# Performance work log

Hardware: AMD Instinct MI355X
Metric: run time of the kernel (lower is better)

The kernel has to match this reference:

```python
import jax, jax.numpy as jnp
import numpy as np

D_MODEL = 1024
EXPAND = 2
D_INNER = EXPAND * D_MODEL          # 2048
D_STATE = 64
NGROUPS = 1
HEADDIM = 128
NHEADS = D_INNER // HEADDIM         # 16
D_CONV = 4
CONV_DIM = D_INNER + 2 * NGROUPS * D_STATE      # 2176
D_IN_PROJ = 2 * D_INNER + 2 * NGROUPS * D_STATE + NHEADS  # 4240
BATCH = 2
SEQLEN = 4096
RMS_EPS = 1e-5


def setup_inputs() -> dict:
    key = jax.random.key(0)
    ks = jax.random.split(key, 8)
    u = jax.random.normal(ks[0], (BATCH, SEQLEN, D_MODEL), jnp.float32)
    in_proj_w = jax.random.normal(ks[1], (D_IN_PROJ, D_MODEL), jnp.float32) * 0.02
    conv_w = jax.random.normal(ks[2], (CONV_DIM, D_CONV), jnp.float32) * 0.2
    conv_b = jax.random.normal(ks[3], (CONV_DIM,), jnp.float32) * 0.1
    dt_bias = jax.random.normal(ks[4], (NHEADS,), jnp.float32) * 0.5
    # A ~ Uniform(1,16), A_log = log(A)  (as in Mamba2 init)
    A_log = jnp.log(jax.random.uniform(ks[5], (NHEADS,), jnp.float32, 1.0, 16.0))
    D = jnp.ones((NHEADS,), jnp.float32)
    rms_w = jnp.ones((D_INNER,), jnp.float32)
    out_w = jax.random.normal(ks[6], (D_MODEL, D_INNER), jnp.float32) * 0.02
    return {"u": u, "in_proj_w": in_proj_w, "conv_w": conv_w, "conv_b": conv_b,
            "dt_bias": dt_bias, "A_log": A_log, "D": D, "rms_w": rms_w, "out_w": out_w}


def reference(u, in_proj_w, conv_w, conv_b, dt_bias, A_log, D, rms_w, out_w):
    Bsz, L, _ = u.shape
    # in_proj: (B,L,d_model) -> (B,L,d_in_proj), split [z, x, B, C, dt]
    zxbcdt = jnp.einsum('bld,ed->ble', u, in_proj_w)
    s1 = D_INNER
    s2 = 2 * D_INNER
    s3 = s2 + NGROUPS * D_STATE
    s4 = s3 + NGROUPS * D_STATE
    z = zxbcdt[..., :s1]
    x = zxbcdt[..., s1:s2]
    B_part = zxbcdt[..., s2:s3]
    C_part = zxbcdt[..., s3:s4]
    dt = zxbcdt[..., s4:]
    dt = jax.nn.softplus(dt + dt_bias)            # (B,L,H), dt_limit=(0,inf) -> no clamp

    # depthwise causal conv1d + silu over [x, B, C]
    xBC = jnp.concatenate([x, B_part, C_part], axis=-1)      # (B,L,CONV_DIM)
    xt = xBC.transpose(0, 2, 1)                              # (B,C,L)
    kern = conv_w[:, None, :]                                # (C,1,W)
    conv = jax.lax.conv_general_dilated(
        xt, kern, (1,), [(D_CONV - 1, 0)],
        dimension_numbers=('NCH', 'OIH', 'NCH'),
        feature_group_count=CONV_DIM)
    xBC = jax.nn.silu((conv + conv_b[None, :, None]).transpose(0, 2, 1))

    x_c = xBC[..., :D_INNER]
    B_c = xBC[..., D_INNER:D_INNER + NGROUPS * D_STATE]
    C_c = xBC[..., D_INNER + NGROUPS * D_STATE:]
    x_s = x_c.reshape(Bsz, L, NHEADS, HEADDIM)               # (B,L,H,P)
    hpg = NHEADS // NGROUPS
    B_full = jnp.repeat(B_c.reshape(Bsz, L, NGROUPS, D_STATE), hpg, axis=2)  # (B,L,H,N)
    C_full = jnp.repeat(C_c.reshape(Bsz, L, NGROUPS, D_STATE), hpg, axis=2)

    A = -jnp.exp(A_log)                                      # (H,)

    def step(state, inp):
        x_t, dt_t, B_t, C_t = inp  # (B,H,P),(B,H),(B,H,N),(B,H,N)
        decay = jnp.exp(dt_t * A)[:, :, None, None]          # (B,H,1,1)
        state = decay * state + B_t[:, :, None, :] * x_t[..., None]  # (B,H,P,N)
        y_t = jnp.einsum('bhpn,bhn->bhp', state, C_t)
        return state, y_t

    init = jnp.zeros((Bsz, NHEADS, HEADDIM, D_STATE), u.dtype)
    xs = (x_s.transpose(1, 0, 2, 3), dt.transpose(1, 0, 2),
          B_full.transpose(1, 0, 2, 3), C_full.transpose(1, 0, 2, 3))
    _, ys = jax.lax.scan(step, init, xs)                     # (L,B,H,P)
    y = ys.transpose(1, 0, 2, 3) + D[None, None, :, None] * x_s

    y_flat = y.reshape(Bsz, L, D_INNER)
    mu = jnp.mean(y_flat * y_flat, axis=-1, keepdims=True)
    y_flat = y_flat * jax.lax.rsqrt(mu + RMS_EPS) * rms_w    # RMSNorm
    y_flat = y_flat * jax.nn.sigmoid(z)                      # gate
    return jnp.einsum('bld,ed->ble', y_flat, out_w)          # out_proj (no bias)
```

## Files before the change

### kernel.cpp

```cpp
#include <hip/hip_runtime.h>
#include <math.h>

#define D_MODEL   1024
#define D_INNER   2048
#define D_STATE   64
#define HEADDIM   128
#define NHEADS    16
#define D_CONV    4
#define BATCH     2
#define SEQLEN    4096
#define RMS_EPS   1e-5f
#define D_IN_PROJ 4240

#define ZX_LD     4224

#define LCHUNK    128
#define NCHUNK    (SEQLEN / LCHUNK)

typedef __attribute__((ext_vector_type(8))) short short8;
typedef __attribute__((ext_vector_type(4))) float f32x4;
typedef _Float16 half8 __attribute__((ext_vector_type(8)));

__device__ __forceinline__ ushort f2bf(float f) {
  unsigned u = __float_as_uint(f);
  u += 0x7fff + ((u >> 16) & 1);
  return (ushort)(u >> 16);
}
__device__ __forceinline__ float bf2f(ushort h) {
  return __uint_as_float(((unsigned)h) << 16);
}
__device__ __forceinline__ ushort f2h(float f) {
  _Float16 h = (_Float16)f;
  ushort u; __builtin_memcpy(&u, &h, 2); return u;
}
__device__ __forceinline__ void ld4(const float* p, float* d) {
  float4 v = *(const float4*)p; d[0] = v.x; d[1] = v.y; d[2] = v.z; d[3] = v.w;
}
__device__ __forceinline__ void ld4b(const ushort* p, float* d) {
  ushort4 v = *(const ushort4*)p;
  d[0] = bf2f(v.x); d[1] = bf2f(v.y); d[2] = bf2f(v.z); d[3] = bf2f(v.w);
}

__device__ __forceinline__ void gl_lds16(const ushort* g, ushort* l) {
  __builtin_amdgcn_global_load_lds(
      (const __attribute__((address_space(1))) unsigned int*)g,
      (__attribute__((address_space(3))) unsigned int*)l, 16, 0, 0);
}

__global__ void cvt_split(const float* __restrict__ w,
                          ushort* __restrict__ hi, ushort* __restrict__ lo, int n4) {
  int i = blockIdx.x * 256 + threadIdx.x;
  if (i >= n4) return;
  float4 v = ((const float4*)w)[i];
  ushort h0 = f2bf(v.x), h1 = f2bf(v.y), h2 = f2bf(v.z), h3 = f2bf(v.w);
  ushort l0 = f2bf(v.x - bf2f(h0)), l1 = f2bf(v.y - bf2f(h1));
  ushort l2 = f2bf(v.z - bf2f(h2)), l3 = f2bf(v.w - bf2f(h3));
  ((ushort4*)hi)[i] = make_ushort4(h0, h1, h2, h3);
  ((ushort4*)lo)[i] = make_ushort4(l0, l1, l2, l3);
}

__global__ void cvt_f16(const float* __restrict__ w, ushort* __restrict__ o, int n4) {
  int i = blockIdx.x * 256 + threadIdx.x;
  if (i >= n4) return;
  float4 v = ((const float4*)w)[i];
  ((ushort4*)o)[i] = make_ushort4(f2h(v.x), f2h(v.y), f2h(v.z), f2h(v.w));
}

template<int BM, int BK, bool ALO, bool OBF16>
__launch_bounds__(256, 3)
__global__ void gemm_bf16p(const ushort* __restrict__ Ah, const ushort* __restrict__ Al,
                           const ushort* __restrict__ Bh, const ushort* __restrict__ Bl,
                           float* __restrict__ C, int ldc,
                           int M, int N, int ldab, int Kslice, int n1term) {
  constexpr int BN = 128;
  constexpr int NQ = BK / 8;
  constexpr int RT = BM / 32;
  constexpr int CT = 4;
  constexpr int KS = BK / 32;

  __shared__ ushort As[ALO ? 2 : 1][BM * BK];
  __shared__ ushort Bs[2][BN * BK];

  const int bn   = blockIdx.x * BN;
  if (bn >= N) return;
  const bool two = (bn >= n1term);
  const int t    = threadIdx.x;
  const int bm   = blockIdx.y * BM;
  const int kz   = blockIdx.z;
  const int kb   = kz * Kslice;
  C += (size_t)kz * M * ldc;
  const int wave = t >> 6, lane = t & 63;
  const int ml   = lane & 15, g4 = lane >> 4;
  const int sw   = ml & (NQ - 1);
  const int wr   = wave & 1, wc = wave >> 1;
  const int r0   = wr * RT * 16, c0 = wc * CT * 16;

  f32x4 acc[RT][CT];
#pragma unroll
  for (int i = 0; i < RT; ++i)
#pragma unroll
    for (int j = 0; j < CT; ++j) acc[i][j] = (f32x4){0.f, 0.f, 0.f, 0.f};

  for (int k0 = kb; k0 < kb + Kslice; k0 += BK) {
    __syncthreads();
#pragma unroll
    for (int ii = 0; ii < BM * NQ / 256; ++ii) {
      int idx = t + ii * 256;
      int row = idx / NQ, qs = idx % NQ;
      int qg  = qs ^ (row & (NQ - 1));
      size_t go = (size_t)(bm + row) * ldab + k0 + qg * 8;
      gl_lds16(Ah + go, &As[0][idx * 8]);
      if (ALO) gl_lds16(Al + go, &As[ALO ? 1 : 0][idx * 8]);
    }
#pragma unroll
    for (int ii = 0; ii < BN * NQ / 256; ++ii) {
      int idx = t + ii * 256;
      int row = idx / NQ, qs = idx % NQ;
      int qg  = qs ^ (row & (NQ - 1));
      size_t go = (size_t)(bn + row) * ldab + k0 + qg * 8;
      gl_lds16(Bh + go, &Bs[0][idx * 8]);
      if (two) gl_lds16(Bl + go, &Bs[1][idx * 8]);
    }
    __syncthreads();

#pragma unroll
    for (int ks = 0; ks < KS; ++ks) {
      const int qA = ((ks * 4 + g4) ^ sw) * 8;
      short8 ah[RT], al[RT], bh[CT], bl[CT];
#pragma unroll
      for (int i = 0; i < RT; ++i) {
        int off = (r0 + i * 16 + ml) * BK + qA;
        ah[i] = *(const short8*)&As[0][off];
        if (ALO) al[i] = *(const short8*)&As[ALO ? 1 : 0][off];
      }
#pragma unroll
      for (int j = 0; j < CT; ++j) {
        int off = (c0 + j * 16 + ml) * BK + qA;
        bh[j] = *(const short8*)&Bs[0][off];
        if (two) bl[j] = *(const short8*)&Bs[1][off];
      }
#pragma unroll
      for (int i = 0; i < RT; ++i)
#pragma unroll
        for (int j = 0; j < CT; ++j) {
          acc[i][j] = __builtin_amdgcn_mfma_f32_16x16x32_bf16(ah[i], bh[j], acc[i][j], 0, 0, 0);
          if (two)
            acc[i][j] = __builtin_amdgcn_mfma_f32_16x16x32_bf16(ah[i], bl[j], acc[i][j], 0, 0, 0);
          if (ALO)
            acc[i][j] = __builtin_amdgcn_mfma_f32_16x16x32_bf16(al[i], bh[j], acc[i][j], 0, 0, 0);
        }
    }
  }

#pragma unroll
  for (int i = 0; i < RT; ++i)
#pragma unroll
    for (int j = 0; j < CT; ++j) {
      int col = bn + c0 + j * 16 + ml;
      if (col < N) {
        int rowb = bm + r0 + i * 16 + g4 * 4;
#pragma unroll
        for (int r = 0; r < 4; ++r) {
          if (OBF16) ((ushort*)C)[(size_t)(rowb + r) * ldc + col] = f2bf(acc[i][j][r]);
          else       C[(size_t)(rowb + r) * ldc + col] = acc[i][j][r];
        }
      }
    }
}

template<int BM, int BK, bool OBF16>
__launch_bounds__(256, 4)
__global__ void gemm_f16(const ushort* __restrict__ Ah, const ushort* __restrict__ Bh,
                         float* __restrict__ C, int ldc,
                         int M, int N, int ldab, int Kslice) {
  constexpr int BN = 128;
  constexpr int NQ = BK / 8;
  constexpr int RT = BM / 32;
  constexpr int CT = 4;
  constexpr int KS = BK / 32;

  __shared__ ushort As[BM * BK];
  __shared__ ushort Bs[BN * BK];

  const int bn   = blockIdx.x * BN;
  if (bn >= N) return;
  const int t    = threadIdx.x;
  const int bm   = blockIdx.y * BM;
  const int kz   = blockIdx.z;
  const int kb   = kz * Kslice;
  C += (size_t)kz * M * ldc;
  const int wave = t >> 6, lane = t & 63;
  const int ml   = lane & 15, g4 = lane >> 4;
  const int sw   = ml & (NQ - 1);
  const int wr   = wave & 1, wc = wave >> 1;
  const int r0   = wr * RT * 16, c0 = wc * CT * 16;

  f32x4 acc[RT][CT];
#pragma unroll
  for (int i = 0; i < RT; ++i)
#pragma unroll
    for (int j = 0; j < CT; ++j) acc[i][j] = (f32x4){0.f, 0.f, 0.f, 0.f};

  for (int k0 = kb; k0 < kb + Kslice; k0 += BK) {
    __syncthreads();
#pragma unroll
    for (int ii = 0; ii < BM * NQ / 256; ++ii) {
      int idx = t + ii * 256;
      int row = idx / NQ, qs = idx % NQ;
      int qg  = qs ^ (row & (NQ - 1));
      size_t go = (size_t)(bm + row) * ldab + k0 + qg * 8;
      gl_lds16(Ah + go, &As[idx * 8]);
    }
#pragma unroll
    for (int ii = 0; ii < BN * NQ / 256; ++ii) {
      int idx = t + ii * 256;
      int row = idx / NQ, qs = idx % NQ;
      int qg  = qs ^ (row & (NQ - 1));
      size_t go = (size_t)(bn + row) * ldab + k0 + qg * 8;
      gl_lds16(Bh + go, &Bs[idx * 8]);
    }
    __syncthreads();

#pragma unroll
    for (int ks = 0; ks < KS; ++ks) {
      const int qA = ((ks * 4 + g4) ^ sw) * 8;
      half8 ah[RT], bh[CT];
#pragma unroll
      for (int i = 0; i < RT; ++i)
        ah[i] = *(const half8*)&As[(r0 + i * 16 + ml) * BK + qA];
#pragma unroll
      for (int j = 0; j < CT; ++j)
        bh[j] = *(const half8*)&Bs[(c0 + j * 16 + ml) * BK + qA];
#pragma unroll
      for (int i = 0; i < RT; ++i)
#pragma unroll
        for (int j = 0; j < CT; ++j)
          acc[i][j] = __builtin_amdgcn_mfma_f32_16x16x32_f16(ah[i], bh[j], acc[i][j], 0, 0, 0);
    }
  }

#pragma unroll
  for (int i = 0; i < RT; ++i)
#pragma unroll
    for (int j = 0; j < CT; ++j) {
      int col = bn + c0 + j * 16 + ml;
      if (col < N) {
        int rowb = bm + r0 + i * 16 + g4 * 4;
#pragma unroll
        for (int r = 0; r < 4; ++r) {
          if (OBF16) ((ushort*)C)[(size_t)(rowb + r) * ldc + col] = f2bf(acc[i][j][r]);
          else       C[(size_t)(rowb + r) * ldc + col] = acc[i][j][r];
        }
      }
    }
}

__global__ void add_out(const float* __restrict__ P, float* __restrict__ out, int n4) {
  int i = blockIdx.x * 256 + threadIdx.x;
  if (i >= n4) return;
  float4 a = ((const float4*)P)[i];
  float4 b = ((const float4*)(P + (size_t)SEQLEN * D_MODEL))[i];
  ((float4*)out)[i] = make_float4(a.x + b.x, a.y + b.y, a.z + b.z, a.w + b.w);
}

__global__ void add_dt(const float* __restrict__ P, float* __restrict__ dtb) {
  int i = blockIdx.x * 256 + threadIdx.x;
  if (i >= SEQLEN * NHEADS / 4) return;
  float4 s = ((const float4*)P)[i];
#pragma unroll
  for (int k = 1; k < 8; ++k) {
    float4 v = ((const float4*)(P + (size_t)k * SEQLEN * NHEADS))[i];
    s.x += v.x; s.y += v.y; s.z += v.z; s.w += v.w;
  }
  ((float4*)dtb)[i] = s;
}


__device__ __forceinline__ void cum_scan(float* cum, float v, int t, float* carry) {
  int lane = t & 63;
#pragma unroll
  for (int off = 1; off < 64; off <<= 1) {
    float o = __shfl_up(v, off);
    if (lane >= off) v += o;
  }
  if (t == 63) *carry = v;
  __syncthreads();
  if (t >= 64 && t < LCHUNK) v += *carry;
  if (t < LCHUNK) cum[t] = v;
  __syncthreads();
}

__device__ __forceinline__ void conv4b(const ushort* __restrict__ zx,
                                       const float* __restrict__ cw,
                                       const float* __restrict__ cb,
                                       int l, int col0, float* outv) {
  const ushort* bp = zx + (size_t)l * ZX_LD + col0;
  float r3[4], r2[4], r1[4], r0[4], bb[4];
  ld4b(bp, r3);
  if (l >= 1) ld4b(bp - ZX_LD, r2);     else { r2[0]=r2[1]=r2[2]=r2[3]=0.f; }
  if (l >= 2) ld4b(bp - 2 * ZX_LD, r1); else { r1[0]=r1[1]=r1[2]=r1[3]=0.f; }
  if (l >= 3) ld4b(bp - 3 * ZX_LD, r0); else { r0[0]=r0[1]=r0[2]=r0[3]=0.f; }
  const int ch = col0 - 2048;
  ld4(cb + ch, bb);
#pragma unroll
  for (int j = 0; j < 4; ++j) {
    float w4[4]; ld4(cw + (ch + j) * 4, w4);
    float a = bb[j];
    a = fmaf(w4[0], r0[j], a);
    a = fmaf(w4[1], r1[j], a);
    a = fmaf(w4[2], r2[j], a);
    a = fmaf(w4[3], r3[j], a);
    outv[j] = a / (1.f + __expf(-a));
  }
}

__launch_bounds__(256, 2)
__global__ void passA_ssd(const ushort* __restrict__ zx,
                          const float* __restrict__ dtb,
                          const float* __restrict__ cw, const float* __restrict__ cb,
                          const float* __restrict__ dt_bias,
                          const float* __restrict__ A_log,
                          float* __restrict__ Sc, float* __restrict__ Pc,
                          float* __restrict__ xconv, float* __restrict__ bconv) {
  const int blk = blockIdx.x;
  const int c   = blk & (NCHUNK - 1);
  const int h   = blk >> 5;
  const int l0  = c * LCHUNK;
  const int t   = threadIdx.x;
  const int wave = t >> 6, lane = t & 63;
  const int ml = lane & 15, g4 = lane >> 4;
  const float Ah = -expf(A_log[h]);

  __shared__ float cum[LCHUNK];
  __shared__ float carry;
  __shared__ ushort Xt[2][LCHUNK * 40];
  __shared__ ushort Bt[2][D_STATE * 40];

  {
    float v = 0.f;
    if (t < LCHUNK) {
      float xv = dtb[(size_t)(l0 + t) * NHEADS + h] + dt_bias[h];
      float sp = (xv > 20.f) ? xv : log1pf(expf(xv));
      v = sp * Ah;
    }
    cum_scan(cum, v, t, &carry);
  }
  const float cend = cum[LCHUNK - 1];

  f32x4 acc[2][4];
#pragma unroll
  for (int i = 0; i < 2; ++i)
#pragma unroll
    for (int j = 0; j < 4; ++j) acc[i][j] = (f32x4){0.f, 0.f, 0.f, 0.f};
  const int p0 = wave * 32;

  for (int slab = 0; slab < 4; ++slab) {
    __syncthreads();
    for (int i = 0; i < 4; ++i) {
      int q = t + i * 256;
      int s = q >> 5, p4 = (q & 31) * 4;
      int l = l0 + slab * 32 + s;
      float xv[4];
      conv4b(zx, cw, cb, l, 2048 + h * HEADDIM + p4, xv);
      *(float4*)(xconv + (size_t)l * D_INNER + h * HEADDIM + p4) =
          make_float4(xv[0], xv[1], xv[2], xv[3]);
#pragma unroll
      for (int j = 0; j < 4; ++j) {
        ushort hh = f2bf(xv[j]);
        Xt[0][(p4 + j) * 40 + s] = hh;
        Xt[1][(p4 + j) * 40 + s] = f2bf(xv[j] - bf2f(hh));
      }
    }
    for (int i = 0; i < 2; ++i) {
      int q = t + i * 256;
      int s = q >> 4, n4 = (q & 15) * 4;
      int l = l0 + slab * 32 + s;
      float wd = __expf(cend - cum[slab * 32 + s]);
      float bv[4];
      conv4b(zx, cw, cb, l, 4096 + n4, bv);
      if (h == 0)
        *(float4*)(bconv + (size_t)l * D_STATE + n4) =
            make_float4(bv[0], bv[1], bv[2], bv[3]);
#pragma unroll
      for (int j = 0; j < 4; ++j) {
        float val = bv[j] * wd;
        ushort hh = f2bf(val);
        Bt[0][(n4 + j) * 40 + s] = hh;
        Bt[1][(n4 + j) * 40 + s] = f2bf(val - bf2f(hh));
      }
    }
    __syncthreads();

    short8 xa_h[2], xa_l[2];
#pragma unroll
    for (int pi = 0; pi < 2; ++pi) {
      int off = (p0 + pi * 16 + ml) * 40 + g4 * 8;
      xa_h[pi] = *(const short8*)&Xt[0][off];
      xa_l[pi] = *(const short8*)&Xt[1][off];
    }
#pragma unroll
    for (int ni = 0; ni < 4; ++ni) {
      int off = (ni * 16 + ml) * 40 + g4 * 8;
      short8 bh = *(const short8*)&Bt[0][off];
      short8 bl = *(const short8*)&Bt[1][off];
#pragma unroll
      for (int pi = 0; pi < 2; ++pi) {
        acc[pi][ni] = __builtin_amdgcn_mfma_f32_16x16x32_bf16(xa_h[pi], bh, acc[pi][ni], 0, 0, 0);
        acc[pi][ni] = __builtin_amdgcn_mfma_f32_16x16x32_bf16(xa_h[pi], bl, acc[pi][ni], 0, 0, 0);
        acc[pi][ni] = __builtin_amdgcn_mfma_f32_16x16x32_bf16(xa_l[pi], bh, acc[pi][ni], 0, 0, 0);
      }
    }
  }

  float* S = Sc + (size_t)blk * (HEADDIM * D_STATE);
#pragma unroll
  for (int pi = 0; pi < 2; ++pi)
#pragma unroll
    for (int ni = 0; ni < 4; ++ni) {
      int n = ni * 16 + ml;
#pragma unroll
      for (int r = 0; r < 4; ++r) {
        int p = p0 + pi * 16 + g4 * 4 + r;
        S[(size_t)p * D_STATE + n] = acc[pi][ni][r];
      }
    }
  if (t == 0) Pc[blk] = __expf(cend);
}

__global__ void scan_passB(float* __restrict__ Sc, const float* __restrict__ Pc) {
  const int h = blockIdx.x;
  const int e = blockIdx.y * 512 + threadIdx.x;
  const size_t hb = (size_t)h * NCHUNK;
  float st = 0.f;
  for (int c = 0; c < NCHUNK; ++c) {
    size_t idx = (hb + c) * (HEADDIM * D_STATE) + e;
    float P = Pc[hb + c];
    float v = Sc[idx];
    Sc[idx] = st;
    st = fmaf(P, st, v);
  }
}

__launch_bounds__(256, 2)
__global__ void passC_ssd(const ushort* __restrict__ zx,
                          const float* __restrict__ dtb,
                          const float* __restrict__ cw, const float* __restrict__ cb,
                          const float* __restrict__ dt_bias,
                          const float* __restrict__ A_log,
                          const float* __restrict__ Dp,
                          const float* __restrict__ Sc,
                          const float* __restrict__ bconv,
                          float* __restrict__ ybuf) {
  const int blk = blockIdx.x;
  const int c   = blk & (NCHUNK - 1);
  const int h   = blk >> 5;
  const int l0  = c * LCHUNK;
  const int t   = threadIdx.x;
  const int wave = t >> 6, lane = t & 63;
  const int ml = lane & 15, g4 = lane >> 4;
  const int t0 = wave * 32;
  const float Ah = -expf(A_log[h]);
  const float Dh = Dp[h];

  __shared__ float cum[LCHUNK];
  __shared__ float carry;
  __shared__ ushort Bsl[2][2][32 * 40];
  __shared__ ushort Msl[2][LCHUNK * 40];
  __shared__ ushort Xt[2][LCHUNK * 40];

  {
    float v = 0.f;
    if (t < LCHUNK) {
      float xv = dtb[(size_t)(l0 + t) * NHEADS + h] + dt_bias[h];
      float sp = (xv > 20.f) ? xv : log1pf(expf(xv));
      v = sp * Ah;
    }
    cum_scan(cum, v, t, &carry);
  }

  short8 c_h[2][2], c_l[2][2];
  {
    ushort* CSh = &Msl[0][0];
    ushort* CSl = &Xt[0][0];
    int row = t >> 1, half = t & 1;
    int l = l0 + row;
    int colbase = 4160 + half * 32;
#pragma unroll
    for (int j0 = 0; j0 < 32; j0 += 4) {
      float cv[4];
      conv4b(zx, cw, cb, l, colbase + j0, cv);
      int colc = half * 32 + j0;
      int quad = colc >> 3;
      int addr = row * 64 + ((quad ^ (row & 7)) << 3) + (colc & 7);
      ushort h0 = f2bf(cv[0]), h1 = f2bf(cv[1]), h2 = f2bf(cv[2]), h3 = f2bf(cv[3]);
      *(ushort4*)&CSh[addr] = make_ushort4(h0, h1, h2, h3);
      *(ushort4*)&CSl[addr] = make_ushort4(
          f2bf(cv[0] - bf2f(h0)), f2bf(cv[1] - bf2f(h1)),
          f2bf(cv[2] - bf2f(h2)), f2bf(cv[3] - bf2f(h3)));
    }
    __syncthreads();
#pragma unroll
    for (int ks = 0; ks < 2; ++ks)
#pragma unroll
      for (int ti = 0; ti < 2; ++ti) {
        int rw = t0 + ti * 16 + ml;
        int ad = rw * 64 + (((ks * 4 + g4) ^ (rw & 7)) << 3);
        c_h[ks][ti] = *(const short8*)&CSh[ad];
        c_l[ks][ti] = *(const short8*)&CSl[ad];
      }
  }

  f32x4 accY[2][8];
#pragma unroll
  for (int i = 0; i < 2; ++i)
#pragma unroll
    for (int j = 0; j < 8; ++j) accY[i][j] = (f32x4){0.f, 0.f, 0.f, 0.f};

  const float* xcv = ybuf;

  for (int slab = 0; slab < 4; ++slab) {
    __syncthreads();
#pragma unroll
    for (int i = 0; i < 2; ++i) {
      int q = t + i * 256;
      int s = q >> 4, n4 = (q & 15) * 4;
      int l = l0 + slab * 32 + s;
      float4 v = *(const float4*)(bconv + (size_t)l * D_STATE + n4);
      float bv[4] = {v.x, v.y, v.z, v.w};
      int ks = n4 >> 5, jj = n4 & 31;
      ushort h0 = f2bf(bv[0]), h1 = f2bf(bv[1]), h2 = f2bf(bv[2]), h3 = f2bf(bv[3]);
      *(ushort4*)&Bsl[ks][0][s * 40 + jj] = make_ushort4(h0, h1, h2, h3);
      *(ushort4*)&Bsl[ks][1][s * 40 + jj] = make_ushort4(
          f2bf(bv[0] - bf2f(h0)), f2bf(bv[1] - bf2f(h1)),
          f2bf(bv[2] - bf2f(h2)), f2bf(bv[3] - bf2f(h3)));
    }
#pragma unroll
    for (int i = 0; i < 4; ++i) {
      int q = t + i * 256;
      int p = q & 127, sg = q >> 7;
      ushort hh[4], ll[4];
#pragma unroll
      for (int j = 0; j < 4; ++j) {
        int l = l0 + slab * 32 + sg * 4 + j;
        float xv = xcv[(size_t)l * D_INNER + h * HEADDIM + p];
        hh[j] = f2bf(xv);
        ll[j] = f2bf(xv - bf2f(hh[j]));
      }
      *(ushort4*)&Xt[0][p * 40 + sg * 4] = make_ushort4(hh[0], hh[1], hh[2], hh[3]);
      *(ushort4*)&Xt[1][p * 40 + sg * 4] = make_ushort4(ll[0], ll[1], ll[2], ll[3]);
    }
    __syncthreads();

    if (wave >= slab) {
      f32x4 g[2][2];
#pragma unroll
      for (int i = 0; i < 2; ++i)
#pragma unroll
        for (int j = 0; j < 2; ++j) g[i][j] = (f32x4){0.f, 0.f, 0.f, 0.f};
#pragma unroll
      for (int ks = 0; ks < 2; ++ks) {
#pragma unroll
        for (int si = 0; si < 2; ++si) {
          int off = (si * 16 + ml) * 40 + g4 * 8;
          short8 bh = *(const short8*)&Bsl[ks][0][off];
          short8 bl = *(const short8*)&Bsl[ks][1][off];
#pragma unroll
          for (int ti = 0; ti < 2; ++ti) {
            g[ti][si] = __builtin_amdgcn_mfma_f32_16x16x32_bf16(c_h[ks][ti], bh, g[ti][si], 0, 0, 0);
            g[ti][si] = __builtin_amdgcn_mfma_f32_16x16x32_bf16(c_h[ks][ti], bl, g[ti][si], 0, 0, 0);
            g[ti][si] = __builtin_amdgcn_mfma_f32_16x16x32_bf16(c_l[ks][ti], bh, g[ti][si], 0, 0, 0);
          }
        }
      }
#pragma unroll
      for (int ti = 0; ti < 2; ++ti)
#pragma unroll
        for (int si = 0; si < 2; ++si) {
          int sl = si * 16 + ml;
          int sg = slab * 32 + sl;
#pragma unroll
          for (int r = 0; r < 4; ++r) {
            int tg = t0 + ti * 16 + g4 * 4 + r;
            float coeff = (sg <= tg) ? __expf(cum[tg] - cum[sg]) : 0.f;
            float val = g[ti][si][r] * coeff + ((sg == tg) ? Dh : 0.f);
            ushort hh = f2bf(val);
            Msl[0][tg * 40 + sl] = hh;
            Msl[1][tg * 40 + sl] = f2bf(val - bf2f(hh));
          }
        }
      asm volatile("s_waitcnt lgkmcnt(0)" ::: "memory");
      short8 ma_h[2], ma_l[2];
#pragma unroll
      for (int ti = 0; ti < 2; ++ti) {
        int off = (t0 + ti * 16 + ml) * 40 + g4 * 8;
        ma_h[ti] = *(const short8*)&Msl[0][off];
        ma_l[ti] = *(const short8*)&Msl[1][off];
      }
#pragma unroll
      for (int pi = 0; pi < 8; ++pi) {
        int off = (pi * 16 + ml) * 40 + g4 * 8;
        short8 xh = *(const short8*)&Xt[0][off];
        short8 xl = *(const short8*)&Xt[1][off];
#pragma unroll
        for (int ti = 0; ti < 2; ++ti) {
          accY[ti][pi] = __builtin_amdgcn_mfma_f32_16x16x32_bf16(ma_h[ti], xh, accY[ti][pi], 0, 0, 0);
          accY[ti][pi] = __builtin_amdgcn_mfma_f32_16x16x32_bf16(ma_h[ti], xl, accY[ti][pi], 0, 0, 0);
          accY[ti][pi] = __builtin_amdgcn_mfma_f32_16x16x32_bf16(ma_l[ti], xh, accY[ti][pi], 0, 0, 0);
        }
      }
    }
  }

  const float* S = Sc + (size_t)blk * (HEADDIM * D_STATE);
#pragma unroll
  for (int ns = 0; ns < 2; ++ns) {
    __syncthreads();
#pragma unroll
    for (int i = 0; i < 4; ++i) {
      int q = t + i * 256;
      int p = q >> 3, j4 = (q & 7) * 4;
      float4 v = *(const float4*)(S + (size_t)p * D_STATE + ns * 32 + j4);
      float vv[4] = {v.x, v.y, v.z, v.w};
      ushort hh0 = f2bf(vv[0]), hh1 = f2bf(vv[1]), hh2 = f2bf(vv[2]), hh3 = f2bf(vv[3]);
      *(ushort4*)&Xt[0][p * 40 + j4] = make_ushort4(hh0, hh1, hh2, hh3);
      *(ushort4*)&Xt[1][p * 40 + j4] =
          make_ushort4(f2bf(vv[0] - bf2f(hh0)), f2bf(vv[1] - bf2f(hh1)),
                       f2bf(vv[2] - bf2f(hh2)), f2bf(vv[3] - bf2f(hh3)));
    }
    __syncthreads();
    short8 ma_h[2], ma_l[2];
#pragma unroll
    for (int ti = 0; ti < 2; ++ti) {
      float e = __expf(cum[t0 + ti * 16 + ml]);
#pragma unroll
      for (int j = 0; j < 8; ++j) {
        float v = (bf2f((ushort)c_h[ns][ti][j]) + bf2f((ushort)c_l[ns][ti][j])) * e;
        ushort hh = f2bf(v);
        ma_h[ti][j] = (short)hh;
        ma_l[ti][j] = (short)f2bf(v - bf2f(hh));
      }
    }
#pragma unroll
    for (int pi = 0; pi < 8; ++pi) {
      int off = (pi * 16 + ml) * 40 + g4 * 8;
      short8 xh = *(const short8*)&Xt[0][off];
      short8 xl = *(const short8*)&Xt[1][off];
#pragma unroll
      for (int ti = 0; ti < 2; ++ti) {
        accY[ti][pi] = __builtin_amdgcn_mfma_f32_16x16x32_bf16(ma_h[ti], xh, accY[ti][pi], 0, 0, 0);
        accY[ti][pi] = __builtin_amdgcn_mfma_f32_16x16x32_bf16(ma_h[ti], xl, accY[ti][pi], 0, 0, 0);
        accY[ti][pi] = __builtin_amdgcn_mfma_f32_16x16x32_bf16(ma_l[ti], xh, accY[ti][pi], 0, 0, 0);
      }
    }
  }

#pragma unroll
  for (int ti = 0; ti < 2; ++ti)
#pragma unroll
    for (int pi = 0; pi < 8; ++pi) {
      int p = pi * 16 + ml;
#pragma unroll
      for (int r = 0; r < 4; ++r) {
        int l = l0 + t0 + ti * 16 + g4 * 4 + r;
        ybuf[(size_t)l * D_INNER + h * HEADDIM + p] = accY[ti][pi][r];
      }
    }
}

__launch_bounds__(256)
__global__ void rmsnorm_gate_split(const float* __restrict__ ybuf,
                                   const ushort* __restrict__ zx,
                                   const float* __restrict__ rms_w,
                                   ushort* __restrict__ yh) {
  const int row = blockIdx.x;
  const int t   = threadIdx.x;
  const float* y  = ybuf + (size_t)row * D_INNER;
  const ushort* z = zx   + (size_t)row * ZX_LD;

  float4 a  = *(const float4*)(y + t * 8);
  float4 bq = *(const float4*)(y + t * 8 + 4);
  float ss = a.x * a.x + a.y * a.y + a.z * a.z + a.w * a.w +
             bq.x * bq.x + bq.y * bq.y + bq.z * bq.z + bq.w * bq.w;
#pragma unroll
  for (int off = 32; off > 0; off >>= 1) ss += __shfl_down(ss, off);
  __shared__ float red[4];
  if ((t & 63) == 0) red[t >> 6] = ss;
  __syncthreads();
  float tot = red[0] + red[1] + red[2] + red[3];
  float scale = rsqrtf(tot * (1.f / (float)D_INNER) + RMS_EPS);

  float vy[8] = {a.x, a.y, a.z, a.w, bq.x, bq.y, bq.z, bq.w};
  ushort4 zv0 = *(const ushort4*)(z + t * 8);
  ushort4 zv1 = *(const ushort4*)(z + t * 8 + 4);
  ushort zz[8] = {zv0.x, zv0.y, zv0.z, zv0.w, zv1.x, zv1.y, zv1.z, zv1.w};
  ushort hh[8];
#pragma unroll
  for (int jj = 0; jj < 8; ++jj) {
    int col = t * 8 + jj;
    float g = 1.f / (1.f + __expf(-bf2f(zz[jj])));
    float v = vy[jj] * scale * rms_w[col] * g;
    hh[jj] = f2h(v);
  }
  size_t o = (size_t)row * D_INNER + t * 8;
  *(ushort4*)(yh + o)     = make_ushort4(hh[0], hh[1], hh[2], hh[3]);
  *(ushort4*)(yh + o + 4) = make_ushort4(hh[4], hh[5], hh[6], hh[7]);
}

extern "C" void kernel_launch(void* const* d_in, const int* in_sizes, int n_in,
                              void* d_out, int out_size, void* d_ws, size_t ws_size,
                              hipStream_t stream) {
  const float* u         = (const float*)d_in[0];
  const float* in_proj_w = (const float*)d_in[1];
  const float* conv_w    = (const float*)d_in[2];
  const float* conv_b    = (const float*)d_in[3];
  const float* dt_bias   = (const float*)d_in[4];
  const float* A_log     = (const float*)d_in[5];
  const float* Dp        = (const float*)d_in[6];
  const float* rms_w     = (const float*)d_in[7];
  const float* out_w     = (const float*)d_in[8];
  float* out = (float*)d_out;

  float* ws    = (float*)d_ws;
  ushort* zxbc = (ushort*)ws;
  float* dtb   = ws   + (size_t)SEQLEN * ZX_LD / 2;
  float* dtp   = dtb  + (size_t)SEQLEN * NHEADS;
  float* ybuf  = dtp  + (size_t)8 * SEQLEN * NHEADS;
  float* Pc    = ybuf + (size_t)SEQLEN * D_INNER;
  float* Sc    = Pc   + 512;
  ushort* uh   = (ushort*)(Sc + (size_t)NHEADS * NCHUNK * HEADDIM * D_STATE);
  ushort* ul   = uh  + (size_t)SEQLEN * D_MODEL;
  ushort* w1h  = ul  + (size_t)SEQLEN * D_MODEL;
  ushort* w1l  = w1h + (size_t)D_IN_PROJ * D_MODEL;
  ushort* w2h  = w1l + (size_t)D_IN_PROJ * D_MODEL;
  ushort* w2l  = w2h + (size_t)D_MODEL * D_INNER;
  ushort* yh   = (ushort*)Sc;
  float* Opart = ybuf;
  float* bconv = dtp;
  ushort* uf16 = (ushort*)ybuf;

  {
    int n4 = D_IN_PROJ * D_MODEL / 4;
    cvt_split<<<(n4 + 255) / 256, 256, 0, stream>>>(in_proj_w, w1h, w1l, n4);
    int z4 = ZX_LD * D_MODEL / 4;
    cvt_f16<<<(z4 + 255) / 256, 256, 0, stream>>>(in_proj_w, w1h, z4);
    int m4 = D_MODEL * D_INNER / 4;
    cvt_f16<<<(m4 + 255) / 256, 256, 0, stream>>>(out_w, w2h, m4);
  }

  for (int b = 0; b < BATCH; ++b) {
    const float* u_b  = u   + (size_t)b * SEQLEN * D_MODEL;
    float*      out_b = out + (size_t)b * SEQLEN * D_MODEL;

    {
      int n4 = SEQLEN * D_MODEL / 4;
      cvt_split<<<(n4 + 255) / 256, 256, 0, stream>>>(u_b, uh, ul, n4);
      cvt_f16<<<(n4 + 255) / 256, 256, 0, stream>>>(u_b, uf16, n4);
    }

    {
      dim3 g(40, SEQLEN / 128, 1);
      gemm_f16<128, 64, true><<<g, 256, 0, stream>>>(uf16, w1h, (float*)zxbc,
                                                     ZX_LD, SEQLEN, ZX_LD,
                                                     D_MODEL, D_MODEL);
    }
    {
      const ushort* bh = w1h + (size_t)ZX_LD * D_MODEL;
      const ushort* bl = w1l + (size_t)ZX_LD * D_MODEL;
      dim3 g(1, SEQLEN / 128, 8);
      gemm_bf16p<128, 32, true, false><<<g, 256, 0, stream>>>(uh, ul, bh, bl,
                                                          dtp, NHEADS, SEQLEN, NHEADS,
                                                          D_MODEL, D_MODEL / 8, 0);
      add_dt<<<(SEQLEN * NHEADS / 4 + 255) / 256, 256, 0, stream>>>(dtp, dtb);
    }

    passA_ssd<<<NHEADS * NCHUNK, 256, 0, stream>>>(zxbc, dtb, conv_w, conv_b,
                                                   dt_bias, A_log, Sc, Pc,
                                                   ybuf, bconv);
    scan_passB<<<dim3(NHEADS, (HEADDIM * D_STATE) / 512), 512, 0, stream>>>(Sc, Pc);
    passC_ssd<<<NHEADS * NCHUNK, 256, 0, stream>>>(zxbc, dtb, conv_w, conv_b,
                                                   dt_bias, A_log, Dp, Sc,
                                                   bconv, ybuf);

    rmsnorm_gate_split<<<SEQLEN, 256, 0, stream>>>(ybuf, zxbc, rms_w, yh);

    {
      dim3 g(D_MODEL / 128, SEQLEN / 128, 2);
      gemm_f16<128, 64, false><<<g, 256, 0, stream>>>(yh, w2h, Opart, D_MODEL,
                                                      SEQLEN, D_MODEL,
                                                      D_INNER, D_INNER / 2);
    }
    add_out<<<(SEQLEN * D_MODEL / 4 + 255) / 256, 256, 0, stream>>>(Opart, out_b,
                                                                    SEQLEN * D_MODEL / 4);
  }
}
```

Before: 518.8 us.

## Double-buffer LDS tiles in f16 GEMM with prefetch two stages ahead

Converts the f16 MFMA GEMM to a double-buffered LDS pipeline. The next k-tile's global-to-LDS loads are issued before computing on the current tile, and manual vmcnt waits plus barriers replace the two per-iteration syncthreads. The goal is to hide global load latency behind MFMA work. In exchange the kernel uses twice the shared memory, and launch bounds are lowered to 2 blocks per CU, which may reduce occupancy. The vmcnt literal assumes exactly 8 loads per stage.

```diff
diff --git a/kernel.cpp b/kernel.cpp
--- a/kernel.cpp
+++ b/kernel.cpp
@@ -169,7 +169,7 @@
 }
 
 template<int BM, int BK, bool OBF16>
-__launch_bounds__(256, 4)
+__launch_bounds__(256, 2)
 __global__ void gemm_f16(const ushort* __restrict__ Ah, const ushort* __restrict__ Bh,
                          float* __restrict__ C, int ldc,
                          int M, int N, int ldab, int Kslice) {
@@ -178,9 +178,10 @@
   constexpr int RT = BM / 32;
   constexpr int CT = 4;
   constexpr int KS = BK / 32;
-
-  __shared__ ushort As[BM * BK];
-  __shared__ ushort Bs[BN * BK];
+  constexpr int LPT = (BM + BN) * NQ / 256;
+
+  __shared__ ushort As[2][BM * BK];
+  __shared__ ushort Bs[2][BN * BK];
 
   const int bn   = blockIdx.x * BN;
   if (bn >= N) return;
@@ -201,15 +202,16 @@
 #pragma unroll
     for (int j = 0; j < CT; ++j) acc[i][j] = (f32x4){0.f, 0.f, 0.f, 0.f};
 
-  for (int k0 = kb; k0 < kb + Kslice; k0 += BK) {
-    __syncthreads();
+  const int NIT = Kslice / BK;
+
+  auto stage = [&](int k0, int buf) {
 #pragma unroll
     for (int ii = 0; ii < BM * NQ / 256; ++ii) {
       int idx = t + ii * 256;
       int row = idx / NQ, qs = idx % NQ;
       int qg  = qs ^ (row & (NQ - 1));
       size_t go = (size_t)(bm + row) * ldab + k0 + qg * 8;
-      gl_lds16(Ah + go, &As[idx * 8]);
+      gl_lds16(Ah + go, &As[buf][idx * 8]);
     }
 #pragma unroll
     for (int ii = 0; ii < BN * NQ / 256; ++ii) {
@@ -217,9 +219,23 @@
       int row = idx / NQ, qs = idx % NQ;
       int qg  = qs ^ (row & (NQ - 1));
       size_t go = (size_t)(bn + row) * ldab + k0 + qg * 8;
-      gl_lds16(Bh + go, &Bs[idx * 8]);
-    }
-    __syncthreads();
+      gl_lds16(Bh + go, &Bs[buf][idx * 8]);
+    }
+  };
+
+  stage(kb, 0);
+  if (NIT > 1) stage(kb + BK, 1);
+
+  for (int it = 0; it < NIT; ++it) {
+    const int buf = it & 1;
+    if (it + 1 < NIT) {
+      static_assert(LPT == 8, "vmcnt literal assumes 8 loads/stage");
+      asm volatile("s_waitcnt vmcnt(8)" ::: "memory");
+    } else {
+      asm volatile("s_waitcnt vmcnt(0)" ::: "memory");
+    }
+    __builtin_amdgcn_s_barrier();
+    __builtin_amdgcn_sched_barrier(0);
 
 #pragma unroll
     for (int ks = 0; ks < KS; ++ks) {
@@ -227,16 +243,21 @@
       half8 ah[RT], bh[CT];
 #pragma unroll
       for (int i = 0; i < RT; ++i)
-        ah[i] = *(const half8*)&As[(r0 + i * 16 + ml) * BK + qA];
+        ah[i] = *(const half8*)&As[buf][(r0 + i * 16 + ml) * BK + qA];
 #pragma unroll
       for (int j = 0; j < CT; ++j)
-        bh[j] = *(const half8*)&Bs[(c0 + j * 16 + ml) * BK + qA];
+        bh[j] = *(const half8*)&Bs[buf][(c0 + j * 16 + ml) * BK + qA];
 #pragma unroll
       for (int i = 0; i < RT; ++i)
 #pragma unroll
         for (int j = 0; j < CT; ++j)
           acc[i][j] = __builtin_amdgcn_mfma_f32_16x16x32_f16(ah[i], bh[j], acc[i][j], 0, 0, 0);
     }
+
+    __builtin_amdgcn_sched_barrier(0);
+    __builtin_amdgcn_s_barrier();
+    __builtin_amdgcn_sched_barrier(0);
+    if (it + 2 < NIT) stage(kb + (it + 2) * BK, buf);
   }
 
 #pragma unroll
```

Result: no change. 515.1 us (-0.7%).
